# Optimization experiments

Hardware: AMD Instinct MI355X
Metric: run time of the kernel (lower is better)

## Reference

```python
import jax, jax.numpy as jnp
import numpy as np

B, C, N, K_CAND, K_TOP = 8, 16, 65536, 10, 4

def setup_inputs() -> dict:
    key = jax.random.key(0)
    k1, k2, k3, k4, k5, k6 = jax.random.split(key, 6)
    scale = 1.0 / np.sqrt(2 * C)  # conv2d default init scale for fan_in=32
    return {
        "original_features": jax.random.normal(k1, (B, C, N), dtype=jnp.float32),
        "sampled_features": jax.random.normal(k2, (B, C, N, K_CAND), dtype=jnp.float32),
        "w1": jax.random.uniform(k3, (2 * C,), jnp.float32, -scale, scale),
        "b1": jax.random.uniform(k4, (), jnp.float32, -scale, scale),
        "w2": jax.random.uniform(k5, (2 * C,), jnp.float32, -scale, scale),
        "b2": jax.random.uniform(k6, (), jnp.float32, -scale, scale),
    }

def reference(original_features, sampled_features, w1, b1, w2, b2):
    # original_features: [B,C,N]; sampled_features: [B,C,N,K_CAND]
    # 1x1 conv over concat([repeated_orig, sampled]) == two channel contractions
    wo1, ws1 = w1[:C], w1[C:]
    # similarity scores: [B,N,K_CAND]
    sim = jax.nn.sigmoid(
        jnp.einsum('bcn,c->bn', original_features, wo1)[:, :, None]
        + jnp.einsum('bcnk,c->bnk', sampled_features, ws1)
        + b1)
    _, topk_idx = jax.lax.top_k(sim, K_TOP)  # [B,N,K_TOP]
    idx = jnp.broadcast_to(topk_idx[:, None, :, :], (sim.shape[0], C, sim.shape[1], K_TOP))
    topk_features = jnp.take_along_axis(sampled_features, idx, axis=-1)  # [B,C,N,K_TOP]
    wo2, ws2 = w2[:C], w2[C:]
    recal = jax.nn.sigmoid(
        jnp.einsum('bcn,c->bn', original_features, wo2)[:, :, None]
        + jnp.einsum('bcnk,c->bnk', topk_features, ws2)
        + b2)  # [B,N,K_TOP]
    summed = jnp.einsum('bcnk,bnk->bcn', topk_features, recal)
    return original_features + summed
```

## Files before the change

### kernel.cpp

```cpp
#include <hip/hip_runtime.h>
#include <math.h>

#define BB 8
#define CC 16
#define NN 65536
#define KC 10
#define KT 4

#define TPTS 64
#define BLK  256

__global__ __launch_bounds__(BLK) void swg_kernel(
    const float* __restrict__ orig,
    const float* __restrict__ samp,
    const float* __restrict__ w1,
    const float* __restrict__ w2,
    const float* __restrict__ b2p,
    float* __restrict__ out)
{
    __shared__ float lds[CC * TPTS * KC];

    const int t = threadIdx.x;
    const int blk = blockIdx.x;
    const int p0 = blk * TPTS;
    const int b  = p0 >> 16;
    const int n0 = p0 & (NN - 1);

    const int q = t & 3;
    const int p = t >> 2;
    const int n = n0 + p;

    float o[4];
#pragma unroll
    for (int cc = 0; cc < 4; ++cc) {
        const int c = q * 4 + cc;
        o[cc] = orig[(size_t)(b * CC + c) * NN + n];
    }

    {
        const int sc = t >> 4;
        const int sl = t & 15;
        const size_t gbase = ((size_t)(b * CC + sc) * NN + n0) * KC;
        const float4* g4 = (const float4*)(samp + gbase);
        float4* l4 = (float4*)(lds + sc * (TPTS * KC));
#pragma unroll
        for (int j = 0; j < 10; ++j)
            l4[j * 16 + sl] = g4[j * 16 + sl];
    }
    __syncthreads();

    const float b2 = b2p[0];

    float ws1[4], wo2[4], ws2[4];
#pragma unroll
    for (int cc = 0; cc < 4; ++cc) {
        const int c = q * 4 + cc;
        ws1[cc] = w1[CC + c];
        wo2[cc] = w2[c];
        ws2[cc] = w2[CC + c];
    }

    float v[4][KC];
#pragma unroll
    for (int cc = 0; cc < 4; ++cc) {
        const int c = q * 4 + cc;
        const float2* lp = (const float2*)(lds + c * (TPTS * KC) + p * KC);
#pragma unroll
        for (int j = 0; j < 5; ++j) {
            const float2 x = lp[j];
            v[cc][2 * j]     = x.x;
            v[cc][2 * j + 1] = x.y;
        }
    }

    float s[KC], d2[KC];
    float dO = 0.f;
#pragma unroll
    for (int k = 0; k < KC; ++k) { s[k] = 0.f; d2[k] = 0.f; }
#pragma unroll
    for (int cc = 0; cc < 4; ++cc) {
        dO += o[cc] * wo2[cc];
#pragma unroll
        for (int k = 0; k < KC; ++k) {
            s[k]  += v[cc][k] * ws1[cc];
            d2[k] += v[cc][k] * ws2[cc];
        }
    }

#pragma unroll
    for (int m = 1; m <= 2; m <<= 1) {
        dO += __shfl_xor(dO, m, 64);
#pragma unroll
        for (int k = 0; k < KC; ++k) {
            s[k]  += __shfl_xor(s[k],  m, 64);
            d2[k] += __shfl_xor(d2[k], m, 64);
        }
    }

    int rank[KC];
#pragma unroll
    for (int k = 0; k < KC; ++k) rank[k] = 0;
#pragma unroll
    for (int j = 0; j < KC; ++j) {
#pragma unroll
        for (int k = j + 1; k < KC; ++k) {
            const bool jge = s[j] >= s[k];
            rank[k] += jge ? 1 : 0;
            rank[j] += jge ? 0 : 1;
        }
    }

    float w[KC];
#pragma unroll
    for (int k = 0; k < KC; ++k) {
        const float x = dO + d2[k] + b2;
        const float sig = __builtin_amdgcn_rcpf(1.f + __expf(-x));
        w[k] = (rank[k] < KT) ? sig : 0.f;
    }

#pragma unroll
    for (int cc = 0; cc < 4; ++cc) {
        float sum = 0.f;
#pragma unroll
        for (int k = 0; k < KC; ++k) sum += v[cc][k] * w[k];
        const int c = q * 4 + cc;
        out[(size_t)(b * CC + c) * NN + n] = o[cc] + sum;
    }
}

extern "C" void kernel_launch(void* const* d_in, const int* in_sizes, int n_in,
                              void* d_out, int out_size, void* d_ws, size_t ws_size,
                              hipStream_t stream) {
    const float* orig = (const float*)d_in[0];
    const float* samp = (const float*)d_in[1];
    const float* w1   = (const float*)d_in[2];
    const float* w2   = (const float*)d_in[4];
    const float* b2   = (const float*)d_in[5];
    float* out = (float*)d_out;

    const int grid = (BB * NN) / TPTS;
    hipLaunchKernelGGL(swg_kernel, dim3(grid), dim3(BLK), 0, stream,
                       orig, samp, w1, w2, b2, out);
}
```

Baseline: 78.36 us.

## Persistent tiles with direct global-to-LDS async loads overlapping compute

Each block now processes eight consecutive 64-point tiles. Sampled features are fetched straight into LDS with global_load_lds, and the next tile's load and orig reads are issued while the current tile is computed, so load latency overlaps compute. The grid shrinks eightfold and launch bounds request 4 blocks per CU. The rank computation is restructured per candidate and fused with the weighted sum. The risks are that a single LDS buffer forces a barrier between reading and refilling, and that fewer blocks give less parallelism to hide memory latency.

```diff
diff --git a/kernel.cpp b/kernel.cpp
--- a/kernel.cpp
+++ b/kernel.cpp
@@ -9,8 +9,12 @@
 
 #define TPTS 64
 #define BLK  256
+#define ITERS 8
 
-__global__ __launch_bounds__(BLK) void swg_kernel(
+typedef __attribute__((address_space(3))) void lds_t;
+typedef __attribute__((address_space(1))) void glob_t;
+
+__global__ __launch_bounds__(BLK, 4) void swg_kernel(
     const float* __restrict__ orig,
     const float* __restrict__ samp,
     const float* __restrict__ w1,
@@ -18,39 +22,31 @@
     const float* __restrict__ b2p,
     float* __restrict__ out)
 {
-    __shared__ float lds[CC * TPTS * KC];
+    __shared__ float4 buf[CC * TPTS * KC / 4];
 
-    const int t = threadIdx.x;
-    const int blk = blockIdx.x;
-    const int p0 = blk * TPTS;
-    const int b  = p0 >> 16;
-    const int n0 = p0 & (NN - 1);
+    const int t   = threadIdx.x;
+    const int bid = blockIdx.x;
+    const int l   = t & 63;
+    const int wid = t >> 6;
+
+    int goff[10];
+#pragma unroll
+    for (int j = 0; j < 10; ++j) {
+        const int idx = wid * 640 + j * 64 + l;
+        const int c   = idx / 160;
+        const int r   = idx - c * 160;
+        goff[j] = c * (NN * KC / 4) + r;
+    }
+    char* lds_base = (char*)buf + wid * 10240;
+
+    const int T0 = bid * ITERS;
+    const int b  = T0 >> 10;
+    const float4* sampB = (const float4*)samp + (size_t)b * (CC * (size_t)NN * KC / 4);
 
     const int q = t & 3;
     const int p = t >> 2;
-    const int n = n0 + p;
-
-    float o[4];
-#pragma unroll
-    for (int cc = 0; cc < 4; ++cc) {
-        const int c = q * 4 + cc;
-        o[cc] = orig[(size_t)(b * CC + c) * NN + n];
-    }
-
-    {
-        const int sc = t >> 4;
-        const int sl = t & 15;
-        const size_t gbase = ((size_t)(b * CC + sc) * NN + n0) * KC;
-        const float4* g4 = (const float4*)(samp + gbase);
-        float4* l4 = (float4*)(lds + sc * (TPTS * KC));
-#pragma unroll
-        for (int j = 0; j < 10; ++j)
-            l4[j * 16 + sl] = g4[j * 16 + sl];
-    }
-    __syncthreads();
 
     const float b2 = b2p[0];
-
     float ws1[4], wo2[4], ws2[4];
 #pragma unroll
     for (int cc = 0; cc < 4; ++cc) {
@@ -60,71 +56,106 @@
         ws2[cc] = w2[CC + c];
     }
 
-    float v[4][KC];
+    {
+        const int n0q = (T0 & 1023) * 160;
 #pragma unroll
-    for (int cc = 0; cc < 4; ++cc) {
-        const int c = q * 4 + cc;
-        const float2* lp = (const float2*)(lds + c * (TPTS * KC) + p * KC);
+        for (int j = 0; j < 10; ++j)
+            __builtin_amdgcn_global_load_lds(
+                (const glob_t*)(sampB + n0q + goff[j]),
+                (lds_t*)(lds_base + j * 1024), 16, 0, 0);
+    }
+    float o[4];
+    {
+        const int n = (T0 & 1023) * 64 + p;
 #pragma unroll
-        for (int j = 0; j < 5; ++j) {
-            const float2 x = lp[j];
-            v[cc][2 * j]     = x.x;
-            v[cc][2 * j + 1] = x.y;
+        for (int cc = 0; cc < 4; ++cc)
+            o[cc] = orig[((size_t)(b * CC + q * 4 + cc)) * NN + n];
+    }
+    asm volatile("s_waitcnt vmcnt(0)\ns_barrier" ::: "memory");
+
+    for (int g = 0; g < ITERS; ++g) {
+        const int T = T0 + g;
+        const int n = (T & 1023) * 64 + p;
+
+        float v[4][KC];
+#pragma unroll
+        for (int cc = 0; cc < 4; ++cc) {
+            const int c = q * 4 + cc;
+            const float2* lp = (const float2*)((const float*)buf + c * (TPTS * KC) + p * KC);
+#pragma unroll
+            for (int j = 0; j < 5; ++j) {
+                const float2 x = lp[j];
+                v[cc][2 * j]     = x.x;
+                v[cc][2 * j + 1] = x.y;
+            }
         }
-    }
+        asm volatile("s_waitcnt lgkmcnt(0)\ns_barrier" ::: "memory");
 
-    float s[KC], d2[KC];
-    float dO = 0.f;
+        float o_nx[4];
+        if (g + 1 < ITERS) {
+            const int Tn  = T + 1;
+            const int n0q = (Tn & 1023) * 160;
 #pragma unroll
-    for (int k = 0; k < KC; ++k) { s[k] = 0.f; d2[k] = 0.f; }
+            for (int j = 0; j < 10; ++j)
+                __builtin_amdgcn_global_load_lds(
+                    (const glob_t*)(sampB + n0q + goff[j]),
+                    (lds_t*)(lds_base + j * 1024), 16, 0, 0);
+            const int nn = (Tn & 1023) * 64 + p;
 #pragma unroll
-    for (int cc = 0; cc < 4; ++cc) {
-        dO += o[cc] * wo2[cc];
+            for (int cc = 0; cc < 4; ++cc)
+                o_nx[cc] = orig[((size_t)(b * CC + q * 4 + cc)) * NN + nn];
+        }
+
+        float s[KC], d2[KC];
+        float dO = 0.f;
+#pragma unroll
+        for (int k = 0; k < KC; ++k) { s[k] = 0.f; d2[k] = 0.f; }
+#pragma unroll
+        for (int cc = 0; cc < 4; ++cc) {
+            dO += o[cc] * wo2[cc];
+#pragma unroll
+            for (int k = 0; k < KC; ++k) {
+                s[k]  += v[cc][k] * ws1[cc];
+                d2[k] += v[cc][k] * ws2[cc];
+            }
+        }
+
+#pragma unroll
+        for (int m = 1; m <= 2; m <<= 1) {
+            dO += __shfl_xor(dO, m, 64);
+#pragma unroll
+            for (int k = 0; k < KC; ++k) {
+                s[k]  += __shfl_xor(s[k],  m, 64);
+                d2[k] += __shfl_xor(d2[k], m, 64);
+            }
+        }
+
+        float sum[4] = {0.f, 0.f, 0.f, 0.f};
 #pragma unroll
         for (int k = 0; k < KC; ++k) {
-            s[k]  += v[cc][k] * ws1[cc];
-            d2[k] += v[cc][k] * ws2[cc];
+            int rk = 0;
+#pragma unroll
+            for (int j = 0; j < KC; ++j) {
+                if (j == k) continue;
+                const bool beats = (j < k) ? (s[j] >= s[k]) : (s[j] > s[k]);
+                rk += beats ? 1 : 0;
+            }
+            const float x  = dO + d2[k] + b2;
+            const float sig = __builtin_amdgcn_rcpf(1.f + __expf(-x));
+            const float wk = (rk < KT) ? sig : 0.f;
+#pragma unroll
+            for (int cc = 0; cc < 4; ++cc) sum[cc] += v[cc][k] * wk;
         }
-    }
 
 #pragma unroll
-    for (int m = 1; m <= 2; m <<= 1) {
-        dO += __shfl_xor(dO, m, 64);
+        for (int cc = 0; cc < 4; ++cc)
+            out[((size_t)(b * CC + q * 4 + cc)) * NN + n] = o[cc] + sum[cc];
+
+        if (g + 1 < ITERS) {
+            asm volatile("s_waitcnt vmcnt(0)\ns_barrier" ::: "memory");
 #pragma unroll
-        for (int k = 0; k < KC; ++k) {
-            s[k]  += __shfl_xor(s[k],  m, 64);
-            d2[k] += __shfl_xor(d2[k], m, 64);
+            for (int cc = 0; cc < 4; ++cc) o[cc] = o_nx[cc];
         }
-    }
-
-    int rank[KC];
-#pragma unroll
-    for (int k = 0; k < KC; ++k) rank[k] = 0;
-#pragma unroll
-    for (int j = 0; j < KC; ++j) {
-#pragma unroll
-        for (int k = j + 1; k < KC; ++k) {
-            const bool jge = s[j] >= s[k];
-            rank[k] += jge ? 1 : 0;
-            rank[j] += jge ? 0 : 1;
-        }
-    }
-
-    float w[KC];
-#pragma unroll
-    for (int k = 0; k < KC; ++k) {
-        const float x = dO + d2[k] + b2;
-        const float sig = __builtin_amdgcn_rcpf(1.f + __expf(-x));
-        w[k] = (rank[k] < KT) ? sig : 0.f;
-    }
-
-#pragma unroll
-    for (int cc = 0; cc < 4; ++cc) {
-        float sum = 0.f;
-#pragma unroll
-        for (int k = 0; k < KC; ++k) sum += v[cc][k] * w[k];
-        const int c = q * 4 + cc;
-        out[(size_t)(b * CC + c) * NN + n] = o[cc] + sum;
     }
 }
 
@@ -138,7 +169,7 @@
     const float* b2   = (const float*)d_in[5];
     float* out = (float*)d_out;
 
-    const int grid = (BB * NN) / TPTS;
+    const int grid = (BB * NN) / (TPTS * ITERS);
     hipLaunchKernelGGL(swg_kernel, dim3(grid), dim3(BLK), 0, stream,
                        orig, samp, w1, w2, b2, out);
 }
```

New measurement: 99.75 us. 27.3% more time.
